# Optimization experiments

Hardware: AMD Instinct MI355X
Metric: run time of the kernel (lower is better)

The kernel has to match this reference:

```python
import jax, jax.numpy as jnp
import numpy as np


def setup_inputs() -> dict:
    key = jax.random.key(0)
    k1, k2 = jax.random.split(key)
    WS, M, K, N = 8, 8192, 512, 1024  # world_size, tokens, local-K, N
    inp = jax.random.normal(k1, (WS, M, K), dtype=jnp.float32)
    weight = jax.random.normal(k2, (WS, N, K), dtype=jnp.float32) * 0.02
    return {"input": inp, "weight": weight}


def reference(input, weight):
    # Per-rank partial GEMM: input [ws, M, K] x weight [ws, N, K] -> [ws, M, N]
    ws, M, _ = input.shape
    N = weight.shape[1]
    Ms = M // ws  # rows per rank after reduce-scatter
    partial = jnp.einsum("wmk,wnk->wmn", input, weight)
    # Reduce-scatter over M dim: rank r receives sum over ranks of rows [r*Ms:(r+1)*Ms]
    # partial -> [src_rank=ws, dst_rank=ws, Ms, N], sum over src_rank
    out = partial.reshape(ws, ws, Ms, N).sum(axis=0)  # [ws, Ms, N]
    return out
```

## Files before the change

### kernel.cpp

```cpp
#include <hip/hip_runtime.h>
#include <hip/hip_bf16.h>


#define WS 8
#define MM 8192
#define KK 512
#define NN 1024
#define KTOT (WS * KK)
#define BM 128
#define BN 128
#define BK 64
#define NBLK ((MM / BM) * (NN / BN))

#define A_ELEMS ((size_t)WS * MM * KK)
#define B_ELEMS ((size_t)WS * NN * KK)
#define WS_NEEDED ((A_ELEMS + B_ELEMS) * 2)

typedef __attribute__((ext_vector_type(8))) short short8;
typedef __attribute__((ext_vector_type(4))) short short4v;
typedef __attribute__((ext_vector_type(4))) float floatx4;

static __device__ inline short f2bf(float f) {
    union { __hip_bfloat16 h; short s; } u;
    u.h = __float2bfloat16(f);
    return u.s;
}

static __device__ inline void glds16(const short* g, short* l) {
    __builtin_amdgcn_global_load_lds(
        (const __attribute__((address_space(1))) unsigned int*)(uintptr_t)g,
        (__attribute__((address_space(3))) unsigned int*)(uintptr_t)l,
        16, 0, 0);
}

#define CVT_ABLOCKS 16384
#define CVT_NBLOCKS 18432

__global__ __launch_bounds__(256)
void cvt_f32_bf16(const float* __restrict__ A, const float* __restrict__ B,
                  short* __restrict__ Abf, short* __restrict__ Bbf) {
    const float* src;
    short* dst;
    size_t base;
    if (blockIdx.x < CVT_ABLOCKS) {
        src = A; dst = Abf;
        base = ((size_t)blockIdx.x * 256 + threadIdx.x) * 8;
    } else {
        src = B; dst = Bbf;
        base = ((size_t)(blockIdx.x - CVT_ABLOCKS) * 256 + threadIdx.x) * 8;
    }
    float4 v0 = *(const float4*)(src + base);
    float4 v1 = *(const float4*)(src + base + 4);
    short8 o = { f2bf(v0.x), f2bf(v0.y), f2bf(v0.z), f2bf(v0.w),
                 f2bf(v1.x), f2bf(v1.y), f2bf(v1.z), f2bf(v1.w) };
    *(short8*)(dst + base) = o;
}

__global__ __launch_bounds__(256, 2)
void gemm_bf16_rs(const short* __restrict__ Abf, const short* __restrict__ Bbf,
                  float* __restrict__ C) {
    __shared__ short As[2][BM * BK];
    __shared__ short Bs[2][BN * BK];

    const int tid  = threadIdx.x;
    const int lane = tid & 63;
    const int wid  = tid >> 6;

    const int lin = blockIdx.y * gridDim.x + blockIdx.x;
    const int T   = (lin & 7) * (NBLK / 8) + (lin >> 3);
    const int ty  = T >> 3;
    const int tx  = T & 7;
    const int m0  = ty * BM;
    const int n0  = tx * BN;

    const int wr = wid >> 1, wc = wid & 1;
    const int lm = lane & 15, quad = lane >> 4;

    const int lrow = lane >> 3;
    const int ss   = (lane & 7) ^ lrow;

    size_t gA[4], gB[4];
#pragma unroll
    for (int t = 0; t < 4; ++t) {
        gA[t] = (size_t)(m0 + wid * 32 + t * 8 + lrow) * KK + ss * 8;
        gB[t] = (size_t)(n0 + wid * 32 + t * 8 + lrow) * KK + ss * 8;
    }

    floatx4 acc[4][4];
#pragma unroll
    for (int i = 0; i < 4; ++i)
#pragma unroll
        for (int j = 0; j < 4; ++j) acc[i][j] = (floatx4)0.f;

    auto stage = [&](int buf, int kt) {
        const int w  = kt >> 9;
        const int kk = kt & (KK - 1);
        const short* Aw = Abf + (size_t)w * MM * KK + kk;
        const short* Bw = Bbf + (size_t)w * NN * KK + kk;
#pragma unroll
        for (int t = 0; t < 4; ++t)
            glds16(Aw + gA[t], &As[buf][(wid * 4 + t) * 512 + lane * 8]);
#pragma unroll
        for (int t = 0; t < 4; ++t)
            glds16(Bw + gB[t], &Bs[buf][(wid * 4 + t) * 512 + lane * 8]);
    };

    stage(0, 0);
    __syncthreads();

    for (int kt = 0; kt < KTOT; kt += BK) {
        const int cur = (kt >> 6) & 1;
        if (kt + BK < KTOT) stage(cur ^ 1, kt + BK);

        short8 af[2][4], bfr[2][4];
#pragma unroll
        for (int kc = 0; kc < 2; ++kc) {
#pragma unroll
            for (int i = 0; i < 4; ++i) {
                const int row = wr * 64 + i * 16 + lm;
                const int sa  = (kc * 4 + quad) ^ (lm & 7);
                af[kc][i] = *(const short8*)&As[cur][row * BK + sa * 8];
            }
#pragma unroll
            for (int j = 0; j < 4; ++j) {
                const int row = wc * 64 + j * 16 + lm;
                const int sb  = (kc * 4 + quad) ^ (lm & 7);
                bfr[kc][j] = *(const short8*)&Bs[cur][row * BK + sb * 8];
            }
        }
        __builtin_amdgcn_s_setprio(1);
#pragma unroll
        for (int kc = 0; kc < 2; ++kc)
#pragma unroll
            for (int i = 0; i < 4; ++i)
#pragma unroll
                for (int j = 0; j < 4; ++j)
                    acc[i][j] = __builtin_amdgcn_mfma_f32_16x16x32_bf16(
                        af[kc][i], bfr[kc][j], acc[i][j], 0, 0, 0);
        __builtin_amdgcn_s_setprio(0);
        __syncthreads();
    }

#pragma unroll
    for (int i = 0; i < 4; ++i)
#pragma unroll
        for (int j = 0; j < 4; ++j) {
            const int n = n0 + wc * 64 + j * 16 + lm;
#pragma unroll
            for (int r = 0; r < 4; ++r) {
                const int m = m0 + wr * 64 + i * 16 + quad * 4 + r;
                C[(size_t)m * NN + n] = acc[i][j][r];
            }
        }
}

__global__ __launch_bounds__(256, 2)
void gemm_rs_fused(const float* __restrict__ A, const float* __restrict__ B,
                   float* __restrict__ C) {
    __shared__ short As[128 * 32];
    __shared__ short Bs[128 * 32];
    const int tid = threadIdx.x;
    const int m0 = blockIdx.y * 128;
    const int n0 = blockIdx.x * 128;
    const int wid = tid >> 6, lane = tid & 63;
    const int wr = wid >> 1, wc = wid & 1;
    const int lm = lane & 15, quad = lane >> 4;
    floatx4 acc[4][4];
#pragma unroll
    for (int i = 0; i < 4; ++i)
#pragma unroll
        for (int j = 0; j < 4; ++j) acc[i][j] = (floatx4)0.f;
    for (int kt = 0; kt < KTOT; kt += 32) {
        const int w = kt >> 9, kk = kt & (KK - 1);
        const float* Aw = A + (size_t)w * MM * KK;
        const float* Bw = B + (size_t)w * NN * KK;
        __syncthreads();
#pragma unroll
        for (int i = 0; i < 4; ++i) {
            const int idx = i * 256 + tid;
            const int row = idx >> 3;
            const int c4 = (idx & 7) * 4;
            float4 av = *(const float4*)&Aw[(size_t)(m0 + row) * KK + kk + c4];
            float4 bv = *(const float4*)&Bw[(size_t)(n0 + row) * KK + kk + c4];
            short4v a4 = { f2bf(av.x), f2bf(av.y), f2bf(av.z), f2bf(av.w) };
            short4v b4 = { f2bf(bv.x), f2bf(bv.y), f2bf(bv.z), f2bf(bv.w) };
            *(short4v*)&As[row * 32 + c4] = a4;
            *(short4v*)&Bs[row * 32 + c4] = b4;
        }
        __syncthreads();
        short8 af[4], bfr[4];
#pragma unroll
        for (int i = 0; i < 4; ++i)
            af[i] = *(const short8*)&As[(wr * 64 + i * 16 + lm) * 32 + quad * 8];
#pragma unroll
        for (int j = 0; j < 4; ++j)
            bfr[j] = *(const short8*)&Bs[(wc * 64 + j * 16 + lm) * 32 + quad * 8];
#pragma unroll
        for (int i = 0; i < 4; ++i)
#pragma unroll
            for (int j = 0; j < 4; ++j)
                acc[i][j] = __builtin_amdgcn_mfma_f32_16x16x32_bf16(
                    af[i], bfr[j], acc[i][j], 0, 0, 0);
    }
#pragma unroll
    for (int i = 0; i < 4; ++i)
#pragma unroll
        for (int j = 0; j < 4; ++j) {
            const int n = n0 + wc * 64 + j * 16 + lm;
#pragma unroll
            for (int r = 0; r < 4; ++r) {
                const int m = m0 + wr * 64 + i * 16 + quad * 4 + r;
                C[(size_t)m * NN + n] = acc[i][j][r];
            }
        }
}

extern "C" void kernel_launch(void* const* d_in, const int* in_sizes, int n_in,
                              void* d_out, int out_size, void* d_ws, size_t ws_size,
                              hipStream_t stream) {
    const float* A = (const float*)d_in[0];
    const float* B = (const float*)d_in[1];
    float* C = (float*)d_out;

    if (ws_size >= WS_NEEDED) {
        short* Abf = (short*)d_ws;
        short* Bbf = Abf + A_ELEMS;
        cvt_f32_bf16<<<CVT_NBLOCKS, 256, 0, stream>>>(A, B, Abf, Bbf);
        dim3 grid(NN / BN, MM / BM);
        gemm_bf16_rs<<<grid, 256, 0, stream>>>(Abf, Bbf, C);
    } else {
        dim3 grid(NN / 128, MM / 128);
        gemm_rs_fused<<<grid, 256, 0, stream>>>(A, B, C);
    }
}
```

Baseline: 272.3 us.

## Fuse fp32-to-bf16 conversion into GEMM with register-prefetched pipeline

Removes the separate conversion kernel and its bf16 workspace round trip. The GEMM now loads fp32 tiles of A and B straight into registers one stage ahead, converts them to bf16, and writes them into the double-buffered LDS tiles. The LDS writes are interleaved with the MFMA loop, replacing the async global-to-LDS loads. This saves a full extra pass over the inputs, but it doubles the bytes per tile load and adds 64 prefetch registers per thread, which risks lower occupancy or spills.

```diff
diff --git a/kernel.cpp b/kernel.cpp
--- a/kernel.cpp
+++ b/kernel.cpp
@@ -12,12 +12,7 @@
 #define BK 64
 #define NBLK ((MM / BM) * (NN / BN))
 
-#define A_ELEMS ((size_t)WS * MM * KK)
-#define B_ELEMS ((size_t)WS * NN * KK)
-#define WS_NEEDED ((A_ELEMS + B_ELEMS) * 2)
-
 typedef __attribute__((ext_vector_type(8))) short short8;
-typedef __attribute__((ext_vector_type(4))) short short4v;
 typedef __attribute__((ext_vector_type(4))) float floatx4;
 
 static __device__ inline short f2bf(float f) {
@@ -26,39 +21,9 @@
     return u.s;
 }
 
-static __device__ inline void glds16(const short* g, short* l) {
-    __builtin_amdgcn_global_load_lds(
-        (const __attribute__((address_space(1))) unsigned int*)(uintptr_t)g,
-        (__attribute__((address_space(3))) unsigned int*)(uintptr_t)l,
-        16, 0, 0);
-}
-
-#define CVT_ABLOCKS 16384
-#define CVT_NBLOCKS 18432
-
-__global__ __launch_bounds__(256)
-void cvt_f32_bf16(const float* __restrict__ A, const float* __restrict__ B,
-                  short* __restrict__ Abf, short* __restrict__ Bbf) {
-    const float* src;
-    short* dst;
-    size_t base;
-    if (blockIdx.x < CVT_ABLOCKS) {
-        src = A; dst = Abf;
-        base = ((size_t)blockIdx.x * 256 + threadIdx.x) * 8;
-    } else {
-        src = B; dst = Bbf;
-        base = ((size_t)(blockIdx.x - CVT_ABLOCKS) * 256 + threadIdx.x) * 8;
-    }
-    float4 v0 = *(const float4*)(src + base);
-    float4 v1 = *(const float4*)(src + base + 4);
-    short8 o = { f2bf(v0.x), f2bf(v0.y), f2bf(v0.z), f2bf(v0.w),
-                 f2bf(v1.x), f2bf(v1.y), f2bf(v1.z), f2bf(v1.w) };
-    *(short8*)(dst + base) = o;
-}
-
 __global__ __launch_bounds__(256, 2)
-void gemm_bf16_rs(const short* __restrict__ Abf, const short* __restrict__ Bbf,
-                  float* __restrict__ C) {
+void gemm_rs_fused2(const float* __restrict__ A, const float* __restrict__ B,
+                    float* __restrict__ C) {
     __shared__ short As[2][BM * BK];
     __shared__ short Bs[2][BN * BK];
 
@@ -77,7 +42,8 @@
     const int lm = lane & 15, quad = lane >> 4;
 
     const int lrow = lane >> 3;
-    const int ss   = (lane & 7) ^ lrow;
+    const int p    = lane & 7;
+    const int ss   = p ^ lrow;
 
     size_t gA[4], gB[4];
 #pragma unroll
@@ -85,6 +51,7 @@
         gA[t] = (size_t)(m0 + wid * 32 + t * 8 + lrow) * KK + ss * 8;
         gB[t] = (size_t)(n0 + wid * 32 + t * 8 + lrow) * KK + ss * 8;
     }
+    const int wbase = wid * 4 * 512 + lane * 8;
 
     floatx4 acc[4][4];
 #pragma unroll
@@ -92,25 +59,44 @@
 #pragma unroll
         for (int j = 0; j < 4; ++j) acc[i][j] = (floatx4)0.f;
 
-    auto stage = [&](int buf, int kt) {
+    float4 ra[4][2], rb[4][2];
+
+    auto LOAD = [&](int kt) {
         const int w  = kt >> 9;
         const int kk = kt & (KK - 1);
-        const short* Aw = Abf + (size_t)w * MM * KK + kk;
-        const short* Bw = Bbf + (size_t)w * NN * KK + kk;
+        const float* Aw = A + (size_t)w * MM * KK + kk;
+        const float* Bw = B + (size_t)w * NN * KK + kk;
 #pragma unroll
-        for (int t = 0; t < 4; ++t)
-            glds16(Aw + gA[t], &As[buf][(wid * 4 + t) * 512 + lane * 8]);
+        for (int t = 0; t < 4; ++t) {
+            ra[t][0] = *(const float4*)(Aw + gA[t]);
+            ra[t][1] = *(const float4*)(Aw + gA[t] + 4);
+            rb[t][0] = *(const float4*)(Bw + gB[t]);
+            rb[t][1] = *(const float4*)(Bw + gB[t] + 4);
+        }
+    };
+    auto WRITE = [&](int buf) {
 #pragma unroll
-        for (int t = 0; t < 4; ++t)
-            glds16(Bw + gB[t], &Bs[buf][(wid * 4 + t) * 512 + lane * 8]);
+        for (int t = 0; t < 4; ++t) {
+            short8 oa = { f2bf(ra[t][0].x), f2bf(ra[t][0].y),
+                          f2bf(ra[t][0].z), f2bf(ra[t][0].w),
+                          f2bf(ra[t][1].x), f2bf(ra[t][1].y),
+                          f2bf(ra[t][1].z), f2bf(ra[t][1].w) };
+            *(short8*)&As[buf][wbase + t * 512] = oa;
+            short8 ob = { f2bf(rb[t][0].x), f2bf(rb[t][0].y),
+                          f2bf(rb[t][0].z), f2bf(rb[t][0].w),
+                          f2bf(rb[t][1].x), f2bf(rb[t][1].y),
+                          f2bf(rb[t][1].z), f2bf(rb[t][1].w) };
+            *(short8*)&Bs[buf][wbase + t * 512] = ob;
+        }
     };
 
-    stage(0, 0);
+    LOAD(0);
+    WRITE(0);
+    LOAD(BK);
     __syncthreads();
 
     for (int kt = 0; kt < KTOT; kt += BK) {
         const int cur = (kt >> 6) & 1;
-        if (kt + BK < KTOT) stage(cur ^ 1, kt + BK);
 
         short8 af[2][4], bfr[2][4];
 #pragma unroll
@@ -128,6 +114,12 @@
                 bfr[kc][j] = *(const short8*)&Bs[cur][row * BK + sb * 8];
             }
         }
+
+        if (kt + BK < KTOT) {
+            WRITE(cur ^ 1);
+            if (kt + 2 * BK < KTOT) LOAD(kt + 2 * BK);
+        }
+
         __builtin_amdgcn_s_setprio(1);
 #pragma unroll
         for (int kc = 0; kc < 2; ++kc)
@@ -154,82 +146,14 @@
         }
 }
 
-__global__ __launch_bounds__(256, 2)
-void gemm_rs_fused(const float* __restrict__ A, const float* __restrict__ B,
-                   float* __restrict__ C) {
-    __shared__ short As[128 * 32];
-    __shared__ short Bs[128 * 32];
-    const int tid = threadIdx.x;
-    const int m0 = blockIdx.y * 128;
-    const int n0 = blockIdx.x * 128;
-    const int wid = tid >> 6, lane = tid & 63;
-    const int wr = wid >> 1, wc = wid & 1;
-    const int lm = lane & 15, quad = lane >> 4;
-    floatx4 acc[4][4];
-#pragma unroll
-    for (int i = 0; i < 4; ++i)
-#pragma unroll
-        for (int j = 0; j < 4; ++j) acc[i][j] = (floatx4)0.f;
-    for (int kt = 0; kt < KTOT; kt += 32) {
-        const int w = kt >> 9, kk = kt & (KK - 1);
-        const float* Aw = A + (size_t)w * MM * KK;
-        const float* Bw = B + (size_t)w * NN * KK;
-        __syncthreads();
-#pragma unroll
-        for (int i = 0; i < 4; ++i) {
-            const int idx = i * 256 + tid;
-            const int row = idx >> 3;
-            const int c4 = (idx & 7) * 4;
-            float4 av = *(const float4*)&Aw[(size_t)(m0 + row) * KK + kk + c4];
-            float4 bv = *(const float4*)&Bw[(size_t)(n0 + row) * KK + kk + c4];
-            short4v a4 = { f2bf(av.x), f2bf(av.y), f2bf(av.z), f2bf(av.w) };
-            short4v b4 = { f2bf(bv.x), f2bf(bv.y), f2bf(bv.z), f2bf(bv.w) };
-            *(short4v*)&As[row * 32 + c4] = a4;
-            *(short4v*)&Bs[row * 32 + c4] = b4;
-        }
-        __syncthreads();
-        short8 af[4], bfr[4];
-#pragma unroll
-        for (int i = 0; i < 4; ++i)
-            af[i] = *(const short8*)&As[(wr * 64 + i * 16 + lm) * 32 + quad * 8];
-#pragma unroll
-        for (int j = 0; j < 4; ++j)
-            bfr[j] = *(const short8*)&Bs[(wc * 64 + j * 16 + lm) * 32 + quad * 8];
-#pragma unroll
-        for (int i = 0; i < 4; ++i)
-#pragma unroll
-            for (int j = 0; j < 4; ++j)
-                acc[i][j] = __builtin_amdgcn_mfma_f32_16x16x32_bf16(
-                    af[i], bfr[j], acc[i][j], 0, 0, 0);
-    }
-#pragma unroll
-    for (int i = 0; i < 4; ++i)
-#pragma unroll
-        for (int j = 0; j < 4; ++j) {
-            const int n = n0 + wc * 64 + j * 16 + lm;
-#pragma unroll
-            for (int r = 0; r < 4; ++r) {
-                const int m = m0 + wr * 64 + i * 16 + quad * 4 + r;
-                C[(size_t)m * NN + n] = acc[i][j][r];
-            }
-        }
-}
-
 extern "C" void kernel_launch(void* const* d_in, const int* in_sizes, int n_in,
                               void* d_out, int out_size, void* d_ws, size_t ws_size,
                               hipStream_t stream) {
     const float* A = (const float*)d_in[0];
     const float* B = (const float*)d_in[1];
     float* C = (float*)d_out;
+    (void)d_ws; (void)ws_size;
 
-    if (ws_size >= WS_NEEDED) {
-        short* Abf = (short*)d_ws;
-        short* Bbf = Abf + A_ELEMS;
-        cvt_f32_bf16<<<CVT_NBLOCKS, 256, 0, stream>>>(A, B, Abf, Bbf);
-        dim3 grid(NN / BN, MM / BM);
-        gemm_bf16_rs<<<grid, 256, 0, stream>>>(Abf, Bbf, C);
-    } else {
-        dim3 grid(NN / 128, MM / 128);
-        gemm_rs_fused<<<grid, 256, 0, stream>>>(A, B, C);
-    }
+    dim3 grid(NN / BN, MM / BM);
+    gemm_rs_fused2<<<grid, 256, 0, stream>>>(A, B, C);
 }
```

Measured after the change: 312.2 us. 14.7% more time.

## Load B fragments directly from global into registers, bypassing LDS

Applied to the files above, without the earlier changes.

The B tile no longer goes through shared memory. Each wave loads its B MFMA fragments straight from global memory into registers, prefetched one K-step ahead and double-buffered in registers with a manually unrolled ping-pong loop. The aim is to halve LDS traffic and LDS footprint. In exchange it adds redundant global/L2 reads of B, since each of the two wave rows reloads the same B data, and raises register pressure from 16 extra short8 prefetch registers, which may hurt occupancy under launch_bounds(256,2).

```diff
diff --git a/kernel.cpp b/kernel.cpp
--- a/kernel.cpp
+++ b/kernel.cpp
@@ -60,7 +60,6 @@
 void gemm_bf16_rs(const short* __restrict__ Abf, const short* __restrict__ Bbf,
                   float* __restrict__ C) {
     __shared__ short As[2][BM * BK];
-    __shared__ short Bs[2][BN * BK];
 
     const int tid  = threadIdx.x;
     const int lane = tid & 63;
@@ -79,12 +78,15 @@
     const int lrow = lane >> 3;
     const int ss   = (lane & 7) ^ lrow;
 
-    size_t gA[4], gB[4];
-#pragma unroll
-    for (int t = 0; t < 4; ++t) {
+    size_t gA[4];
+#pragma unroll
+    for (int t = 0; t < 4; ++t)
         gA[t] = (size_t)(m0 + wid * 32 + t * 8 + lrow) * KK + ss * 8;
-        gB[t] = (size_t)(n0 + wid * 32 + t * 8 + lrow) * KK + ss * 8;
-    }
+
+    size_t gB[4];
+#pragma unroll
+    for (int j = 0; j < 4; ++j)
+        gB[j] = (size_t)(n0 + wc * 64 + j * 16 + lm) * KK + quad * 8;
 
     floatx4 acc[4][4];
 #pragma unroll
@@ -92,42 +94,39 @@
 #pragma unroll
         for (int j = 0; j < 4; ++j) acc[i][j] = (floatx4)0.f;
 
-    auto stage = [&](int buf, int kt) {
+    auto stageA = [&](int buf, int kt) {
         const int w  = kt >> 9;
         const int kk = kt & (KK - 1);
         const short* Aw = Abf + (size_t)w * MM * KK + kk;
-        const short* Bw = Bbf + (size_t)w * NN * KK + kk;
 #pragma unroll
         for (int t = 0; t < 4; ++t)
             glds16(Aw + gA[t], &As[buf][(wid * 4 + t) * 512 + lane * 8]);
-#pragma unroll
-        for (int t = 0; t < 4; ++t)
-            glds16(Bw + gB[t], &Bs[buf][(wid * 4 + t) * 512 + lane * 8]);
     };
-
-    stage(0, 0);
-    __syncthreads();
-
-    for (int kt = 0; kt < KTOT; kt += BK) {
-        const int cur = (kt >> 6) & 1;
-        if (kt + BK < KTOT) stage(cur ^ 1, kt + BK);
-
-        short8 af[2][4], bfr[2][4];
-#pragma unroll
-        for (int kc = 0; kc < 2; ++kc) {
+    auto loadB = [&](short8 (&pre)[2][4], int kt) {
+        const int w  = kt >> 9;
+        const int kk = kt & (KK - 1);
+        const short* Bw = Bbf + (size_t)w * NN * KK + kk;
+#pragma unroll
+        for (int kc = 0; kc < 2; ++kc)
+#pragma unroll
+            for (int j = 0; j < 4; ++j)
+                pre[kc][j] = *(const short8*)(Bw + gB[j] + kc * 32);
+    };
+
+    auto iter = [&](int kt, int cur, short8 (&use)[2][4], short8 (&pre)[2][4]) {
+        if (kt + BK < KTOT) {
+            stageA(cur ^ 1, kt + BK);
+            loadB(pre, kt + BK);
+        }
+        short8 af[2][4];
+#pragma unroll
+        for (int kc = 0; kc < 2; ++kc)
 #pragma unroll
             for (int i = 0; i < 4; ++i) {
                 const int row = wr * 64 + i * 16 + lm;
                 const int sa  = (kc * 4 + quad) ^ (lm & 7);
                 af[kc][i] = *(const short8*)&As[cur][row * BK + sa * 8];
             }
-#pragma unroll
-            for (int j = 0; j < 4; ++j) {
-                const int row = wc * 64 + j * 16 + lm;
-                const int sb  = (kc * 4 + quad) ^ (lm & 7);
-                bfr[kc][j] = *(const short8*)&Bs[cur][row * BK + sb * 8];
-            }
-        }
         __builtin_amdgcn_s_setprio(1);
 #pragma unroll
         for (int kc = 0; kc < 2; ++kc)
@@ -136,9 +135,26 @@
 #pragma unroll
                 for (int j = 0; j < 4; ++j)
                     acc[i][j] = __builtin_amdgcn_mfma_f32_16x16x32_bf16(
-                        af[kc][i], bfr[kc][j], acc[i][j], 0, 0, 0);
+                        af[kc][i], use[kc][j], acc[i][j], 0, 0, 0);
         __builtin_amdgcn_s_setprio(0);
+        if (kt + BK < KTOT) {
+#pragma unroll
+            for (int kc = 0; kc < 2; ++kc)
+#pragma unroll
+                for (int j = 0; j < 4; ++j)
+                    asm volatile("" : "+v"(pre[kc][j]));
+        }
         __syncthreads();
+    };
+
+    short8 bA[2][4], bB[2][4];
+    loadB(bA, 0);
+    stageA(0, 0);
+    __syncthreads();
+
+    for (int kt = 0; kt < KTOT; kt += 2 * BK) {
+        iter(kt,      0, bA, bB);
+        iter(kt + BK, 1, bB, bA);
     }
 
 #pragma unroll
```

Result: slower. 346.9 us (+27.4%).

## Use 256x128 tiles with 512 threads and intra-block split-K reduction

Applied to the files above, without the earlier changes.

Doubles the M tile to 256 and launches 512 threads per block. Wave pairs split each BK=64 step along K, so each wave does 8x4 MFMAs over half the K chunk, and the two halves are summed through LDS at the end. The larger tile is meant to cut global and LDS traffic per FLOP by reusing B across more rows. In exchange it raises accumulator register pressure, adds an epilogue reduction through shared memory, and halves the number of blocks in the grid.

```diff
diff --git a/kernel.cpp b/kernel.cpp
--- a/kernel.cpp
+++ b/kernel.cpp
@@ -7,7 +7,7 @@
 #define KK 512
 #define NN 1024
 #define KTOT (WS * KK)
-#define BM 128
+#define BM 256
 #define BN 128
 #define BK 64
 #define NBLK ((MM / BM) * (NN / BN))
@@ -56,7 +56,7 @@
     *(short8*)(dst + base) = o;
 }
 
-__global__ __launch_bounds__(256, 2)
+__global__ __launch_bounds__(512, 2)
 void gemm_bf16_rs(const short* __restrict__ Abf, const short* __restrict__ Bbf,
                   float* __restrict__ C) {
     __shared__ short As[2][BM * BK];
@@ -73,22 +73,23 @@
     const int m0  = ty * BM;
     const int n0  = tx * BN;
 
-    const int wr = wid >> 1, wc = wid & 1;
+    const int wr = (wid >> 2) & 1, wc = (wid >> 1) & 1, kg = wid & 1;
     const int lm = lane & 15, quad = lane >> 4;
 
     const int lrow = lane >> 3;
     const int ss   = (lane & 7) ^ lrow;
 
-    size_t gA[4], gB[4];
-#pragma unroll
-    for (int t = 0; t < 4; ++t) {
+    size_t gA[4], gB[2];
+#pragma unroll
+    for (int t = 0; t < 4; ++t)
         gA[t] = (size_t)(m0 + wid * 32 + t * 8 + lrow) * KK + ss * 8;
-        gB[t] = (size_t)(n0 + wid * 32 + t * 8 + lrow) * KK + ss * 8;
-    }
-
-    floatx4 acc[4][4];
-#pragma unroll
-    for (int i = 0; i < 4; ++i)
+#pragma unroll
+    for (int t = 0; t < 2; ++t)
+        gB[t] = (size_t)(n0 + wid * 16 + t * 8 + lrow) * KK + ss * 8;
+
+    floatx4 acc[8][4];
+#pragma unroll
+    for (int i = 0; i < 8; ++i)
 #pragma unroll
         for (int j = 0; j < 4; ++j) acc[i][j] = (floatx4)0.f;
 
@@ -101,8 +102,8 @@
         for (int t = 0; t < 4; ++t)
             glds16(Aw + gA[t], &As[buf][(wid * 4 + t) * 512 + lane * 8]);
 #pragma unroll
-        for (int t = 0; t < 4; ++t)
-            glds16(Bw + gB[t], &Bs[buf][(wid * 4 + t) * 512 + lane * 8]);
+        for (int t = 0; t < 2; ++t)
+            glds16(Bw + gB[t], &Bs[buf][(wid * 2 + t) * 512 + lane * 8]);
     };
 
     stage(0, 0);
@@ -112,46 +113,73 @@
         const int cur = (kt >> 6) & 1;
         if (kt + BK < KTOT) stage(cur ^ 1, kt + BK);
 
-        short8 af[2][4], bfr[2][4];
-#pragma unroll
-        for (int kc = 0; kc < 2; ++kc) {
-#pragma unroll
-            for (int i = 0; i < 4; ++i) {
-                const int row = wr * 64 + i * 16 + lm;
-                const int sa  = (kc * 4 + quad) ^ (lm & 7);
-                af[kc][i] = *(const short8*)&As[cur][row * BK + sa * 8];
-            }
-#pragma unroll
-            for (int j = 0; j < 4; ++j) {
-                const int row = wc * 64 + j * 16 + lm;
-                const int sb  = (kc * 4 + quad) ^ (lm & 7);
-                bfr[kc][j] = *(const short8*)&Bs[cur][row * BK + sb * 8];
-            }
-        }
+        short8 af[8], bfr[4];
+        const int sk = (kg * 4 + quad);
+#pragma unroll
+        for (int i = 0; i < 8; ++i) {
+            const int row = wr * 128 + i * 16 + lm;
+            af[i] = *(const short8*)&As[cur][row * BK + (sk ^ (lm & 7)) * 8];
+        }
+#pragma unroll
+        for (int j = 0; j < 4; ++j) {
+            const int row = wc * 64 + j * 16 + lm;
+            bfr[j] = *(const short8*)&Bs[cur][row * BK + (sk ^ (lm & 7)) * 8];
+        }
+
         __builtin_amdgcn_s_setprio(1);
 #pragma unroll
-        for (int kc = 0; kc < 2; ++kc)
-#pragma unroll
-            for (int i = 0; i < 4; ++i)
-#pragma unroll
-                for (int j = 0; j < 4; ++j)
-                    acc[i][j] = __builtin_amdgcn_mfma_f32_16x16x32_bf16(
-                        af[kc][i], bfr[kc][j], acc[i][j], 0, 0, 0);
+        for (int i = 0; i < 8; ++i)
+#pragma unroll
+            for (int j = 0; j < 4; ++j)
+                acc[i][j] = __builtin_amdgcn_mfma_f32_16x16x32_bf16(
+                    af[i], bfr[j], acc[i][j], 0, 0, 0);
         __builtin_amdgcn_s_setprio(0);
         __syncthreads();
     }
 
-#pragma unroll
-    for (int i = 0; i < 4; ++i)
-#pragma unroll
-        for (int j = 0; j < 4; ++j) {
-            const int n = n0 + wc * 64 + j * 16 + lm;
-#pragma unroll
-            for (int r = 0; r < 4; ++r) {
-                const int m = m0 + wr * 64 + i * 16 + quad * 4 + r;
-                C[(size_t)m * NN + n] = acc[i][j][r];
-            }
-        }
+    {
+        float* S = (float*)As;
+        const int slot = wid >> 1;
+#pragma unroll
+        for (int half = 0; half < 2; ++half) {
+            __syncthreads();
+            if (kg == 1) {
+#pragma unroll
+                for (int ii = 0; ii < 4; ++ii)
+#pragma unroll
+                    for (int j = 0; j < 4; ++j)
+#pragma unroll
+                        for (int r = 0; r < 4; ++r)
+                            S[slot * 4096 + (ii * 16 + j * 4 + r) * 64 + lane]
+                                = acc[half * 4 + ii][j][r];
+            }
+            __syncthreads();
+            if (kg == 0) {
+#pragma unroll
+                for (int ii = 0; ii < 4; ++ii)
+#pragma unroll
+                    for (int j = 0; j < 4; ++j)
+#pragma unroll
+                        for (int r = 0; r < 4; ++r)
+                            acc[half * 4 + ii][j][r] +=
+                                S[slot * 4096 + (ii * 16 + j * 4 + r) * 64 + lane];
+            }
+        }
+    }
+
+    if (kg == 0) {
+#pragma unroll
+        for (int i = 0; i < 8; ++i)
+#pragma unroll
+            for (int j = 0; j < 4; ++j) {
+                const int n = n0 + wc * 64 + j * 16 + lm;
+#pragma unroll
+                for (int r = 0; r < 4; ++r) {
+                    const int m = m0 + wr * 128 + i * 16 + quad * 4 + r;
+                    C[(size_t)m * NN + n] = acc[i][j][r];
+                }
+            }
+    }
 }
 
 __global__ __launch_bounds__(256, 2)
@@ -227,7 +255,7 @@
         short* Bbf = Abf + A_ELEMS;
         cvt_f32_bf16<<<CVT_NBLOCKS, 256, 0, stream>>>(A, B, Abf, Bbf);
         dim3 grid(NN / BN, MM / BM);
-        gemm_bf16_rs<<<grid, 256, 0, stream>>>(Abf, Bbf, C);
+        gemm_bf16_rs<<<grid, 512, 0, stream>>>(Abf, Bbf, C);
     } else {
         dim3 grid(NN / 128, MM / 128);
         gemm_rs_fused<<<grid, 256, 0, stream>>>(A, B, C);
```

After: 273.7 us. No clear change (+0.5%).
